# Optimization experiments

Measured on AMD Instinct MI355X. Metric: run time of the kernel, lower is better.

Reference implementation:

```python
import jax, jax.numpy as jnp
import numpy as np

TEMPERATURE = 1.0          # args.matching_temperature default
CONSISTENCY_WEIGHT = 0.5   # args.matching_consistency_weight default
EPS = 1e-6


def setup_inputs() -> dict:
    key = jax.random.key(0)
    k1, k2, k3 = jax.random.split(key, 3)
    query = jax.random.normal(k1, (8192, 1024), dtype=jnp.float32)
    memory_bank = jax.random.normal(k2, (16384, 1024), dtype=jnp.float32)
    # per-memory-entry local density scale (mean kNN distance within the lib)
    neighbor_scale_bank = jax.random.uniform(k3, (16384,), dtype=jnp.float32) + 0.5
    return {
        "query": query,
        "memory_bank": memory_bank,
        "neighbor_scale_bank": neighbor_scale_bank,
        "k": 5,
    }


def _cdist(x, y):
    # Euclidean pairwise distances [Nq, Nm], GEMM-based like torch.cdist.
    x2 = jnp.sum(x * x, axis=1, keepdims=True)          # [Nq, 1]
    y2 = jnp.sum(y * y, axis=1)[None, :]                # [1, Nm]
    d2 = x2 + y2 - 2.0 * (x @ y.T)                      # [Nq, Nm]
    return jnp.sqrt(jnp.maximum(d2, 1e-12))


def reference(query, memory_bank, neighbor_scale_bank, k):
    # _compute_memory_matching_scores with matching_mode='adaptive_knn'
    dist = _cdist(query, memory_bank)                   # [Nq, Nm]
    k = min(k, memory_bank.shape[0])
    neg_d, knn_indices = jax.lax.top_k(-dist, k)        # k smallest distances
    knn_distances = -neg_d                              # [Nq, k]

    # _reduce_knn_distances, mode='adaptive_knn'
    weights = jax.nn.softmax(-knn_distances / TEMPERATURE, axis=1)
    weighted_distance = jnp.sum(weights * knn_distances, axis=1)  # [Nq]

    neighbor_scale = neighbor_scale_bank[knn_indices].mean(axis=1)  # [Nq]
    normalized_distance = weighted_distance / jnp.maximum(neighbor_scale, EPS)

    mean_d = knn_distances.mean(axis=1)
    consistency = knn_distances.std(axis=1) / jnp.maximum(mean_d, EPS)
    return normalized_distance * (1.0 + CONSISTENCY_WEIGHT * consistency)
```

## Files before the change

### kernel.cpp

```cpp
#include <hip/hip_runtime.h>
#include <hip/hip_bf16.h>
#include <math.h>

#define NQ   8192
#define NM   16384
#define DIM  1024
#define KNN  5

#define SPLITS 8
#define SLICE  (NM / SPLITS)
#define TILEM  128
#define TILES  (SLICE / TILEM)
#define BK     64
#define KSTEPS (DIM / BK)
#define UNITS  (TILES * KSTEPS)
#define TPB1   512
#define CPQ    (SPLITS * 16 * 5)

typedef float  f32x4_t  __attribute__((ext_vector_type(4)));
typedef __bf16 bf16x8_t __attribute__((ext_vector_type(8)));

typedef __attribute__((address_space(1))) unsigned int gu32_t;
typedef __attribute__((address_space(3))) unsigned int lu32_t;

__device__ __forceinline__ void gl16(const void* g, void* l) {
    __builtin_amdgcn_global_load_lds((gu32_t*)g, (lu32_t*)l, 16, 0, 0);
}

__global__ void m2_kernel(const float* __restrict__ mem, float* __restrict__ m2) {
    const int row  = blockIdx.x * 4 + (threadIdx.x >> 6);
    const int lane = threadIdx.x & 63;
    const float4* p = reinterpret_cast<const float4*>(mem + (size_t)row * DIM) + lane;
    float s = 0.f;
#pragma unroll
    for (int i = 0; i < 4; ++i) {
        const float4 v = p[i * 64];
        s += v.x * v.x + v.y * v.y + v.z * v.z + v.w * v.w;
    }
#pragma unroll
    for (int off = 32; off > 0; off >>= 1) s += __shfl_down(s, off);
    if (lane == 0) m2[row] = s;
}

__global__ void cvt_bf16_kernel(const float* __restrict__ in,
                                __hip_bfloat16* __restrict__ out, int n8) {
    const int i = blockIdx.x * blockDim.x + threadIdx.x;
    if (i >= n8) return;
    const float4 a = reinterpret_cast<const float4*>(in)[2 * i];
    const float4 b = reinterpret_cast<const float4*>(in)[2 * i + 1];
    bf16x8_t v;
    v[0] = (__bf16)a.x; v[1] = (__bf16)a.y; v[2] = (__bf16)a.z; v[3] = (__bf16)a.w;
    v[4] = (__bf16)b.x; v[5] = (__bf16)b.y; v[6] = (__bf16)b.z; v[7] = (__bf16)b.w;
    reinterpret_cast<bf16x8_t*>(out)[i] = v;
}

__launch_bounds__(TPB1, 4)
__global__ void knn_phase1(const __hip_bfloat16* __restrict__ Qbf,
                           const __hip_bfloat16* __restrict__ Mbf,
                           const float* __restrict__ m2,
                           float* __restrict__ keyws,
                           unsigned short* __restrict__ idxws) {
    __shared__ alignas(16) __bf16 As[2][TILEM][BK];
    __shared__ alignas(16) __bf16 Bs[2][128][BK];
    __shared__ float m2s[SLICE];

    const int t    = threadIdx.x;
    const int lane = t & 63;
    const int wave = t >> 6;
    const int wr   = wave >> 1;
    const int wc   = wave & 1;
    const int g4   = lane >> 4;
    const int l16  = lane & 15;

    const int bid  = blockIdx.x;
    const int qlow = bid & 7;
    const int rest = bid >> 3;
    const int sp   = rest & 7;
    const int qhi  = rest >> 3;
    const int qc   = qhi * 8 + qlow;
    const int q0   = qc * 128;
    const int mbase = sp * SLICE;

#pragma unroll
    for (int i = 0; i < SLICE / TPB1; ++i) m2s[t + i * TPB1] = m2[mbase + t + i * TPB1];

    float    tk[4][5];
    unsigned ti[4][5];
#pragma unroll
    for (int j = 0; j < 4; ++j)
#pragma unroll
        for (int r = 0; r < 5; ++r) { tk[j][r] = 3.4e38f; ti[j][r] = 0u; }

    const int srow = t >> 3;
    const int scol = (((t & 7) ^ (srow & 7)) << 3);
    const int rxa  = l16 & 7;

    f32x4_t acc[2][4];
#pragma unroll
    for (int i = 0; i < 2; ++i)
#pragma unroll
        for (int j = 0; j < 4; ++j) acc[i][j] = {0.f, 0.f, 0.f, 0.f};

    auto stage = [&](int s, int buf) {
        const int tl  = s >> 4;
        const int kk0 = (s & 15) * BK;
        const int rr0 = mbase + tl * TILEM;
        const __hip_bfloat16* ga = Mbf + (size_t)(rr0 + srow) * DIM + kk0 + scol;
        const __hip_bfloat16* gb = Qbf + (size_t)(q0 + srow) * DIM + kk0 + scol;
        char* la = (char*)&As[buf][0][0] + t * 16;
        char* lb = (char*)&Bs[buf][0][0] + t * 16;
        gl16(ga,            la);
        gl16(ga + 64 * DIM, la + 8192);
        gl16(gb,            lb);
        gl16(gb + 64 * DIM, lb + 8192);
    };

    stage(0, 0);
    stage(1, 1);

#pragma unroll 1
    for (int s = 0; s < UNITS; ++s) {
        const int cur = s & 1;

        if (s == UNITS - 1) asm volatile("s_waitcnt vmcnt(0)" ::: "memory");
        else                asm volatile("s_waitcnt vmcnt(4)" ::: "memory");
        __builtin_amdgcn_s_barrier();

        __builtin_amdgcn_s_setprio(1);
#pragma unroll
        for (int kk = 0; kk < BK; kk += 32) {
            const int ch   = (kk >> 3) + g4;
            const int koff = ((ch ^ rxa) << 3);
            const int ar   = wr * 32 + l16;
            const int bc   = wc * 64 + l16;
            const bf16x8_t a0 = *reinterpret_cast<const bf16x8_t*>(&As[cur][ar][koff]);
            const bf16x8_t a1 = *reinterpret_cast<const bf16x8_t*>(&As[cur][ar + 16][koff]);
            const bf16x8_t b0 = *reinterpret_cast<const bf16x8_t*>(&Bs[cur][bc][koff]);
            const bf16x8_t b1 = *reinterpret_cast<const bf16x8_t*>(&Bs[cur][bc + 16][koff]);
            const bf16x8_t b2 = *reinterpret_cast<const bf16x8_t*>(&Bs[cur][bc + 32][koff]);
            const bf16x8_t b3 = *reinterpret_cast<const bf16x8_t*>(&Bs[cur][bc + 48][koff]);
            acc[0][0] = __builtin_amdgcn_mfma_f32_16x16x32_bf16(a0, b0, acc[0][0], 0, 0, 0);
            acc[0][1] = __builtin_amdgcn_mfma_f32_16x16x32_bf16(a0, b1, acc[0][1], 0, 0, 0);
            acc[0][2] = __builtin_amdgcn_mfma_f32_16x16x32_bf16(a0, b2, acc[0][2], 0, 0, 0);
            acc[0][3] = __builtin_amdgcn_mfma_f32_16x16x32_bf16(a0, b3, acc[0][3], 0, 0, 0);
            acc[1][0] = __builtin_amdgcn_mfma_f32_16x16x32_bf16(a1, b0, acc[1][0], 0, 0, 0);
            acc[1][1] = __builtin_amdgcn_mfma_f32_16x16x32_bf16(a1, b1, acc[1][1], 0, 0, 0);
            acc[1][2] = __builtin_amdgcn_mfma_f32_16x16x32_bf16(a1, b2, acc[1][2], 0, 0, 0);
            acc[1][3] = __builtin_amdgcn_mfma_f32_16x16x32_bf16(a1, b3, acc[1][3], 0, 0, 0);
        }
        __builtin_amdgcn_s_setprio(0);

        asm volatile("s_waitcnt lgkmcnt(0)" ::: "memory");
        __builtin_amdgcn_s_barrier();

        if (s + 2 < UNITS) stage(s + 2, cur);

        if ((s & 15) == 15) {
            const int tl = s >> 4;
            const int r0 = mbase + tl * TILEM;
#pragma unroll
            for (int i = 0; i < 2; ++i) {
#pragma unroll
                for (int rg = 0; rg < 4; ++rg) {
                    const int lr = wr * 32 + i * 16 + g4 * 4 + rg;
                    const float mm = m2s[tl * TILEM + lr];
                    const unsigned gidx = (unsigned)(r0 + lr);
#pragma unroll
                    for (int j = 0; j < 4; ++j) {
                        const float key = fmaf(-2.0f, acc[i][j][rg], mm);
                        if (key < tk[j][4]) {
                            tk[j][4] = key; ti[j][4] = gidx;
#pragma unroll
                            for (int ss = 3; ss >= 0; --ss) {
                                const bool sw = tk[j][ss] > tk[j][ss + 1];
                                const float    fa = tk[j][ss], fb = tk[j][ss + 1];
                                const unsigned ia = ti[j][ss], ib = ti[j][ss + 1];
                                tk[j][ss] = sw ? fb : fa; tk[j][ss + 1] = sw ? fa : fb;
                                ti[j][ss] = sw ? ib : ia; ti[j][ss + 1] = sw ? ia : ib;
                            }
                        }
                    }
                }
            }
#pragma unroll
            for (int i = 0; i < 2; ++i)
#pragma unroll
                for (int j = 0; j < 4; ++j) acc[i][j] = {0.f, 0.f, 0.f, 0.f};
        }
    }

#pragma unroll
    for (int j = 0; j < 4; ++j) {
        const int col = wc * 64 + j * 16 + l16;
        const size_t base = (size_t)(q0 + col) * CPQ + sp * 80 + (wr * 4 + g4) * 5;
#pragma unroll
        for (int r = 0; r < 5; ++r) {
            keyws[base + r] = tk[j][r];
            idxws[base + r] = (unsigned short)ti[j][r];
        }
    }
}

__global__ void knn_phase2(const float* __restrict__ query,
                           const float* __restrict__ mem,
                           const float* __restrict__ nsb,
                           const float* __restrict__ keyws,
                           const unsigned short* __restrict__ idxws,
                           float* __restrict__ out) {
    const int wv   = threadIdx.x >> 6;
    const int lane = threadIdx.x & 63;
    const int row  = blockIdx.x * 4 + wv;

    __shared__ int   sel[4][16];
    __shared__ float dsel[4][16];

    float    k[10];
    unsigned id[10];
    const size_t cb = (size_t)row * CPQ;
#pragma unroll
    for (int r = 0; r < 10; ++r) {
        k[r]  = keyws[cb + r * 64 + lane];
        id[r] = (unsigned)idxws[cb + r * 64 + lane];
    }

    for (int rr = 0; rr < 16; ++rr) {
        float lm = k[0];
#pragma unroll
        for (int r = 1; r < 10; ++r) lm = fminf(lm, k[r]);
        float m = lm;
#pragma unroll
        for (int off = 32; off > 0; off >>= 1) m = fminf(m, __shfl_xor(m, off));
        const unsigned long long bal = __ballot(lm == m);
        const bool win = (lane == (int)(__ffsll((long long)bal) - 1));
        unsigned sid = 0; bool done = false;
#pragma unroll
        for (int r = 0; r < 10; ++r) {
            const bool c = win && !done && (k[r] == m);
            sid  = c ? id[r] : sid;
            k[r] = c ? 3.4e38f : k[r];
            done = done || c;
        }
        if (win) sel[wv][rr] = (int)sid;
    }
    __syncthreads();

    const int c = lane >> 2, sub = lane & 3;
    const int mi = sel[wv][c];
    const float4* qp = reinterpret_cast<const float4*>(query + (size_t)row * DIM) + sub * 64;
    const float4* mp = reinterpret_cast<const float4*>(mem + (size_t)mi * DIM) + sub * 64;
    double acc = 0.0;
#pragma unroll 4
    for (int i = 0; i < 64; ++i) {
        const float4 q4 = qp[i];
        const float4 m4 = mp[i];
        const double d0 = (double)q4.x - (double)m4.x;
        const double d1 = (double)q4.y - (double)m4.y;
        const double d2 = (double)q4.z - (double)m4.z;
        const double d3 = (double)q4.w - (double)m4.w;
        acc += d0 * d0 + d1 * d1 + d2 * d2 + d3 * d3;
    }
    acc += __shfl_xor(acc, 1);
    acc += __shfl_xor(acc, 2);
    if (sub == 0) dsel[wv][c] = (float)sqrt(fmax(acc, 1e-12));
    __syncthreads();

    if (lane == 0) {
        float dv[16]; int di[16];
#pragma unroll
        for (int i = 0; i < 16; ++i) { dv[i] = dsel[wv][i]; di[i] = sel[wv][i]; }
        float kd[KNN]; int ki[KNN];
#pragma unroll
        for (int r = 0; r < KNN; ++r) {
            float bv = 3.4e38f; int bi = 0x7fffffff; int bp = -1;
#pragma unroll
            for (int i = 0; i < 16; ++i) {
                const bool better = (dv[i] < bv) || (dv[i] == bv && di[i] < bi);
                if (better) { bv = dv[i]; bi = di[i]; bp = i; }
            }
            kd[r] = bv; ki[r] = bi;
#pragma unroll
            for (int i = 0; i < 16; ++i) if (i == bp) dv[i] = 3.4e38f;
        }
        double dmin = (double)kd[0];
#pragma unroll
        for (int r = 1; r < KNN; ++r) dmin = fmin(dmin, (double)kd[r]);
        double w[KNN], se = 0.0, wd = 0.0, sd = 0.0, sc = 0.0;
#pragma unroll
        for (int r = 0; r < KNN; ++r) {
            w[r] = exp(-((double)kd[r] - dmin));
            se += w[r];
            sd += (double)kd[r];
            sc += (double)nsb[ki[r]];
        }
#pragma unroll
        for (int r = 0; r < KNN; ++r) wd += w[r] * (double)kd[r];
        wd /= se;
        sc /= (double)KNN;
        const double nd   = wd / fmax(sc, 1e-6);
        const double mean = sd / (double)KNN;
        double var = 0.0;
#pragma unroll
        for (int r = 0; r < KNN; ++r) { const double dd = (double)kd[r] - mean; var += dd * dd; }
        var /= (double)KNN;
        const double cons = sqrt(var) / fmax(mean, 1e-6);
        out[row] = (float)(nd * (1.0 + 0.5 * cons));
    }
}

__launch_bounds__(512, 1)
__global__ void fb_knn_phase1(const float* __restrict__ query,
                              const float* __restrict__ mem,
                              const float* __restrict__ m2,
                              float* __restrict__ wkey,
                              int* __restrict__ widx) {
    __shared__ alignas(16) __bf16 Qs[128][72];
    __shared__ alignas(16) __bf16 Ms[128][72];
    __shared__ float D2[128][129];
    __shared__ float m2s[128];

    const int t    = threadIdx.x;
    const int lane = t & 63;
    const int wave = t >> 6;
    const int wr   = wave >> 1;
    const int wc   = wave & 1;

    const int mb    = blockIdx.x & 63;
    const int sp    = blockIdx.x >> 6;
    const int q0    = mb * 128;
    const int mbase = sp * 4096;

    const int srow = t & 127;
    const int sseg = t >> 7;
    const int str = t >> 2;
    const int stc = (t & 3) * 16;

    float topv[8]; int topi[8];
#pragma unroll
    for (int i = 0; i < 8; ++i) { topv[i] = 3.4e38f; topi[i] = 0; }
    float curmax = 3.4e38f;
    const f32x4_t zero = {0.f, 0.f, 0.f, 0.f};

    for (int tile = 0; tile < 32; ++tile) {
        const int c0 = mbase + tile * 128;
        if (t < 128) m2s[t] = m2[c0 + t];
        f32x4_t acc[2][4];
#pragma unroll
        for (int i = 0; i < 2; ++i)
#pragma unroll
            for (int j = 0; j < 4; ++j) acc[i][j] = zero;

        for (int k0 = 0; k0 < DIM; k0 += 64) {
            {
                const float4* qp = reinterpret_cast<const float4*>(query + (size_t)(q0 + str) * DIM + k0 + stc);
                const float4 a0 = qp[0], a1 = qp[1], a2 = qp[2], a3 = qp[3];
                const float4* mp = reinterpret_cast<const float4*>(mem + (size_t)(c0 + str) * DIM + k0 + stc);
                const float4 b0 = mp[0], b1 = mp[1], b2 = mp[2], b3 = mp[3];
                bf16x8_t qa, qb, ma, mbv;
                qa[0] = (__bf16)a0.x; qa[1] = (__bf16)a0.y; qa[2] = (__bf16)a0.z; qa[3] = (__bf16)a0.w;
                qa[4] = (__bf16)a1.x; qa[5] = (__bf16)a1.y; qa[6] = (__bf16)a1.z; qa[7] = (__bf16)a1.w;
                qb[0] = (__bf16)a2.x; qb[1] = (__bf16)a2.y; qb[2] = (__bf16)a2.z; qb[3] = (__bf16)a2.w;
                qb[4] = (__bf16)a3.x; qb[5] = (__bf16)a3.y; qb[6] = (__bf16)a3.z; qb[7] = (__bf16)a3.w;
                ma[0] = (__bf16)b0.x; ma[1] = (__bf16)b0.y; ma[2] = (__bf16)b0.z; ma[3] = (__bf16)b0.w;
                ma[4] = (__bf16)b1.x; ma[5] = (__bf16)b1.y; ma[6] = (__bf16)b1.z; ma[7] = (__bf16)b1.w;
                mbv[0] = (__bf16)b2.x; mbv[1] = (__bf16)b2.y; mbv[2] = (__bf16)b2.z; mbv[3] = (__bf16)b2.w;
                mbv[4] = (__bf16)b3.x; mbv[5] = (__bf16)b3.y; mbv[6] = (__bf16)b3.z; mbv[7] = (__bf16)b3.w;
                *reinterpret_cast<bf16x8_t*>(&Qs[str][stc])     = qa;
                *reinterpret_cast<bf16x8_t*>(&Qs[str][stc + 8]) = qb;
                *reinterpret_cast<bf16x8_t*>(&Ms[str][stc])     = ma;
                *reinterpret_cast<bf16x8_t*>(&Ms[str][stc + 8]) = mbv;
            }
            __syncthreads();
#pragma unroll
            for (int kk = 0; kk < 64; kk += 32) {
                const int koff = kk + ((lane >> 4) << 3);
                const int ar   = wr * 32 + (lane & 15);
                const bf16x8_t a0 = *reinterpret_cast<const bf16x8_t*>(&Qs[ar][koff]);
                const bf16x8_t a1 = *reinterpret_cast<const bf16x8_t*>(&Qs[ar + 16][koff]);
                const int bc = wc * 64 + (lane & 15);
                const bf16x8_t b0 = *reinterpret_cast<const bf16x8_t*>(&Ms[bc][koff]);
                const bf16x8_t b1 = *reinterpret_cast<const bf16x8_t*>(&Ms[bc + 16][koff]);
                const bf16x8_t b2 = *reinterpret_cast<const bf16x8_t*>(&Ms[bc + 32][koff]);
                const bf16x8_t b3 = *reinterpret_cast<const bf16x8_t*>(&Ms[bc + 48][koff]);
                acc[0][0] = __builtin_amdgcn_mfma_f32_16x16x32_bf16(a0, b0, acc[0][0], 0, 0, 0);
                acc[0][1] = __builtin_amdgcn_mfma_f32_16x16x32_bf16(a0, b1, acc[0][1], 0, 0, 0);
                acc[0][2] = __builtin_amdgcn_mfma_f32_16x16x32_bf16(a0, b2, acc[0][2], 0, 0, 0);
                acc[0][3] = __builtin_amdgcn_mfma_f32_16x16x32_bf16(a0, b3, acc[0][3], 0, 0, 0);
                acc[1][0] = __builtin_amdgcn_mfma_f32_16x16x32_bf16(a1, b0, acc[1][0], 0, 0, 0);
                acc[1][1] = __builtin_amdgcn_mfma_f32_16x16x32_bf16(a1, b1, acc[1][1], 0, 0, 0);
                acc[1][2] = __builtin_amdgcn_mfma_f32_16x16x32_bf16(a1, b2, acc[1][2], 0, 0, 0);
                acc[1][3] = __builtin_amdgcn_mfma_f32_16x16x32_bf16(a1, b3, acc[1][3], 0, 0, 0);
            }
            __syncthreads();
        }
#pragma unroll
        for (int i = 0; i < 2; ++i) {
            const int r0 = wr * 32 + i * 16 + ((lane >> 4) << 2);
#pragma unroll
            for (int j = 0; j < 4; ++j) {
                const int cc = wc * 64 + j * 16 + (lane & 15);
                const float mm = m2s[cc];
#pragma unroll
                for (int rg = 0; rg < 4; ++rg)
                    D2[r0 + rg][cc] = mm - 2.0f * acc[i][j][rg];
            }
        }
        __syncthreads();
        {
            const int gbase = c0 + sseg * 32;
#pragma unroll 8
            for (int cc = 0; cc < 32; ++cc) {
                const float key = D2[srow][sseg * 32 + cc];
                if (key < curmax) {
                    bool done = false;
#pragma unroll
                    for (int i = 0; i < 8; ++i) {
                        if (!done && topv[i] == curmax) {
                            topv[i] = key; topi[i] = gbase + cc; done = true;
                        }
                    }
                    curmax = topv[0];
#pragma unroll
                    for (int i = 1; i < 8; ++i) curmax = fmaxf(curmax, topv[i]);
                }
            }
        }
        __syncthreads();
    }
    const size_t base = ((size_t)(q0 + srow) * 4 + sp) * 32 + (size_t)sseg * 8;
#pragma unroll
    for (int j = 0; j < 8; ++j) { wkey[base + j] = topv[j]; widx[base + j] = topi[j]; }
}

__global__ void fb_knn_phase2(const float* __restrict__ query,
                              const float* __restrict__ mem,
                              const float* __restrict__ nsb,
                              const float* __restrict__ wkey,
                              const int* __restrict__ widx,
                              float* __restrict__ out) {
    const int wv   = threadIdx.x >> 6;
    const int lane = threadIdx.x & 63;
    const int row  = blockIdx.x * 4 + wv;
    __shared__ int   sel[4][16];
    __shared__ float dsel[4][16];

    const size_t cb = (size_t)row * 128;
    float k0 = wkey[cb + lane];
    float k1 = wkey[cb + 64 + lane];
    const int i0 = widx[cb + lane];
    const int i1 = widx[cb + 64 + lane];

    for (int r = 0; r < 16; ++r) {
        float m = fminf(k0, k1);
#pragma unroll
        for (int off = 32; off > 0; off >>= 1) m = fminf(m, __shfl_xor(m, off));
        const unsigned long long b0 = __ballot(k0 == m);
        const unsigned long long b1 = __ballot(k1 == m);
        if (b0) {
            if (lane == __ffsll(b0) - 1) { sel[wv][r] = i0; k0 = 3.4e38f; }
        } else {
            if (lane == __ffsll(b1) - 1) { sel[wv][r] = i1; k1 = 3.4e38f; }
        }
    }
    __syncthreads();

    const int c = lane >> 2, sub = lane & 3;
    const int mi = sel[wv][c];
    const float4* qp = reinterpret_cast<const float4*>(query + (size_t)row * DIM) + sub * 64;
    const float4* mp = reinterpret_cast<const float4*>(mem + (size_t)mi * DIM) + sub * 64;
    double acc = 0.0;
#pragma unroll 4
    for (int i = 0; i < 64; ++i) {
        const float4 q4 = qp[i];
        const float4 m4 = mp[i];
        const double d0 = (double)q4.x - (double)m4.x;
        const double d1 = (double)q4.y - (double)m4.y;
        const double d2 = (double)q4.z - (double)m4.z;
        const double d3 = (double)q4.w - (double)m4.w;
        acc += d0 * d0 + d1 * d1 + d2 * d2 + d3 * d3;
    }
    acc += __shfl_xor(acc, 1);
    acc += __shfl_xor(acc, 2);
    if (sub == 0) dsel[wv][c] = (float)sqrt(fmax(acc, 1e-12));
    __syncthreads();

    if (lane == 0) {
        float dv[16]; int di[16];
#pragma unroll
        for (int i = 0; i < 16; ++i) { dv[i] = dsel[wv][i]; di[i] = sel[wv][i]; }
        float kd[KNN]; int ki[KNN];
#pragma unroll
        for (int r = 0; r < KNN; ++r) {
            float bv = 3.4e38f; int bi = 0x7fffffff; int bp = -1;
#pragma unroll
            for (int i = 0; i < 16; ++i) {
                const bool better = (dv[i] < bv) || (dv[i] == bv && di[i] < bi);
                if (better) { bv = dv[i]; bi = di[i]; bp = i; }
            }
            kd[r] = bv; ki[r] = bi;
#pragma unroll
            for (int i = 0; i < 16; ++i) if (i == bp) dv[i] = 3.4e38f;
        }
        double dmin = (double)kd[0];
#pragma unroll
        for (int r = 1; r < KNN; ++r) dmin = fmin(dmin, (double)kd[r]);
        double w[KNN], se = 0.0, wd = 0.0, sd = 0.0, sc = 0.0;
#pragma unroll
        for (int r = 0; r < KNN; ++r) {
            w[r] = exp(-((double)kd[r] - dmin));
            se += w[r];
            sd += (double)kd[r];
            sc += (double)nsb[ki[r]];
        }
#pragma unroll
        for (int r = 0; r < KNN; ++r) wd += w[r] * (double)kd[r];
        wd /= se;
        sc /= (double)KNN;
        const double nd   = wd / fmax(sc, 1e-6);
        const double mean = sd / (double)KNN;
        double var = 0.0;
#pragma unroll
        for (int r = 0; r < KNN; ++r) { const double dd = (double)kd[r] - mean; var += dd * dd; }
        var /= (double)KNN;
        const double cons = sqrt(var) / fmax(mean, 1e-6);
        out[row] = (float)(nd * (1.0 + 0.5 * cons));
    }
}

extern "C" void kernel_launch(void* const* d_in, const int* in_sizes, int n_in,
                              void* d_out, int out_size, void* d_ws, size_t ws_size,
                              hipStream_t stream) {
    const float* query = (const float*)d_in[0];
    const float* mem   = (const float*)d_in[1];
    const float* nsb   = (const float*)d_in[2];
    float* out = (float*)d_out;
    char* ws = (char*)d_ws;

    const size_t offQ   = 0;
    const size_t offM   = offQ + (size_t)NQ * DIM * 2;
    const size_t offm2  = offM + (size_t)NM * DIM * 2;
    const size_t offkey = offm2 + (size_t)NM * 4;
    const size_t offidx = offkey + (size_t)NQ * CPQ * 4;
    const size_t need   = offidx + (size_t)NQ * CPQ * 2;

    if (ws_size >= need) {
        __hip_bfloat16* Qbf = (__hip_bfloat16*)(ws + offQ);
        __hip_bfloat16* Mbf = (__hip_bfloat16*)(ws + offM);
        float*          m2  = (float*)(ws + offm2);
        float*          key = (float*)(ws + offkey);
        unsigned short* idx = (unsigned short*)(ws + offidx);

        hipLaunchKernelGGL(cvt_bf16_kernel, dim3(NQ * DIM / 8 / 256), dim3(256), 0, stream,
                           query, Qbf, NQ * DIM / 8);
        hipLaunchKernelGGL(cvt_bf16_kernel, dim3(NM * DIM / 8 / 256), dim3(256), 0, stream,
                           mem, Mbf, NM * DIM / 8);
        hipLaunchKernelGGL(m2_kernel, dim3(NM / 4), dim3(256), 0, stream, mem, m2);
        hipLaunchKernelGGL(knn_phase1, dim3((NQ / 128) * SPLITS), dim3(TPB1), 0, stream,
                           Qbf, Mbf, m2, key, idx);
        hipLaunchKernelGGL(knn_phase2, dim3(NQ / 4), dim3(256), 0, stream,
                           query, mem, nsb, key, idx, out);
    } else {
        float* wkey = (float*)ws;
        int*   widx = (int*)(ws + (size_t)NQ * 128 * 4);
        float* m2   = (float*)(ws + (size_t)NQ * 128 * 8);
        hipLaunchKernelGGL(m2_kernel, dim3(NM / 4), dim3(256), 0, stream, mem, m2);
        hipLaunchKernelGGL(fb_knn_phase1, dim3((NQ / 128) * 4), dim3(512), 0, stream,
                           query, mem, m2, wkey, widx);
        hipLaunchKernelGGL(fb_knn_phase2, dim3(NQ / 4), dim3(256), 0, stream,
                           query, mem, nsb, wkey, widx, out);
    }
}
```

Measured before the change: 494.9 us.

## Enlarge kNN GEMM block tile to 256x256 and fuse bf16 convert with norms

Phase 1 block tile grows from 128x128 to 256x256, with each wave now computing 128x64 (8x4 MFMA fragments). This raises arithmetic intensity per LDS byte and halves the global reloads of Q and M. The per-query candidate count shrinks accordingly, and phase 2 merges 5 instead of 10 candidates per lane. Separately, the memory-bank bf16 conversion and the squared-norm computation are fused into one kernel so the bank is read once. The cost is more registers, with launch bounds lowered to 2 blocks per CU, double the LDS, and fewer blocks in the grid (256), which may underfill the 256 CUs.

```diff
diff --git a/kernel.cpp b/kernel.cpp
--- a/kernel.cpp
+++ b/kernel.cpp
@@ -9,13 +9,14 @@
 
 #define SPLITS 8
 #define SLICE  (NM / SPLITS)
-#define TILEM  128
-#define TILES  (SLICE / TILEM)
+#define BM     256
+#define BN     256
+#define TILES  (SLICE / BM)
 #define BK     64
 #define KSTEPS (DIM / BK)
 #define UNITS  (TILES * KSTEPS)
 #define TPB1   512
-#define CPQ    (SPLITS * 16 * 5)
+#define CPQ    (SPLITS * 8 * 5)
 
 typedef float  f32x4_t  __attribute__((ext_vector_type(4)));
 typedef __bf16 bf16x8_t __attribute__((ext_vector_type(8)));
@@ -27,15 +28,23 @@
     __builtin_amdgcn_global_load_lds((gu32_t*)g, (lu32_t*)l, 16, 0, 0);
 }
 
-__global__ void m2_kernel(const float* __restrict__ mem, float* __restrict__ m2) {
+__global__ void cvt_m2_kernel(const float* __restrict__ mem,
+                              __hip_bfloat16* __restrict__ out,
+                              float* __restrict__ m2) {
     const int row  = blockIdx.x * 4 + (threadIdx.x >> 6);
     const int lane = threadIdx.x & 63;
-    const float4* p = reinterpret_cast<const float4*>(mem + (size_t)row * DIM) + lane;
+    const float4* p = reinterpret_cast<const float4*>(mem + (size_t)row * DIM + lane * 16);
     float s = 0.f;
 #pragma unroll
-    for (int i = 0; i < 4; ++i) {
-        const float4 v = p[i * 64];
-        s += v.x * v.x + v.y * v.y + v.z * v.z + v.w * v.w;
+    for (int h = 0; h < 2; ++h) {
+        const float4 a = p[2 * h];
+        const float4 b = p[2 * h + 1];
+        bf16x8_t v;
+        v[0] = (__bf16)a.x; v[1] = (__bf16)a.y; v[2] = (__bf16)a.z; v[3] = (__bf16)a.w;
+        v[4] = (__bf16)b.x; v[5] = (__bf16)b.y; v[6] = (__bf16)b.z; v[7] = (__bf16)b.w;
+        reinterpret_cast<bf16x8_t*>(out + (size_t)row * DIM + lane * 16)[h] = v;
+        s += a.x * a.x + a.y * a.y + a.z * a.z + a.w * a.w;
+        s += b.x * b.x + b.y * b.y + b.z * b.z + b.w * b.w;
     }
 #pragma unroll
     for (int off = 32; off > 0; off >>= 1) s += __shfl_down(s, off);
@@ -54,35 +63,39 @@
     reinterpret_cast<bf16x8_t*>(out)[i] = v;
 }
 
-__launch_bounds__(TPB1, 4)
+__launch_bounds__(TPB1, 2)
 __global__ void knn_phase1(const __hip_bfloat16* __restrict__ Qbf,
                            const __hip_bfloat16* __restrict__ Mbf,
                            const float* __restrict__ m2,
                            float* __restrict__ keyws,
                            unsigned short* __restrict__ idxws) {
-    __shared__ alignas(16) __bf16 As[2][TILEM][BK];
-    __shared__ alignas(16) __bf16 Bs[2][128][BK];
+    __shared__ alignas(16) __bf16 As[2][BM][BK];
+    __shared__ alignas(16) __bf16 Bs[2][BN][BK];
     __shared__ float m2s[SLICE];
 
     const int t    = threadIdx.x;
     const int lane = t & 63;
     const int wave = t >> 6;
-    const int wr   = wave >> 1;
-    const int wc   = wave & 1;
+    const int wb   = wave >> 2;
+    const int cb   = wave & 3;
     const int g4   = lane >> 4;
     const int l16  = lane & 15;
 
     const int bid  = blockIdx.x;
-    const int qlow = bid & 7;
-    const int rest = bid >> 3;
-    const int sp   = rest & 7;
-    const int qhi  = rest >> 3;
-    const int qc   = qhi * 8 + qlow;
-    const int q0   = qc * 128;
+    const int sp   = bid & 7;
+    const int qc   = bid >> 3;
+    const int q0   = qc * BN;
     const int mbase = sp * SLICE;
 
-#pragma unroll
-    for (int i = 0; i < SLICE / TPB1; ++i) m2s[t + i * TPB1] = m2[mbase + t + i * TPB1];
+    {
+        float m2r[SLICE / TPB1];
+#pragma unroll
+        for (int i = 0; i < SLICE / TPB1; ++i) m2r[i] = m2[mbase + t + i * TPB1];
+        asm volatile("s_waitcnt vmcnt(0)" ::: "memory");
+#pragma unroll
+        for (int i = 0; i < SLICE / TPB1; ++i) m2s[t + i * TPB1] = m2r[i];
+        __syncthreads();
+    }
 
     float    tk[4][5];
     unsigned ti[4][5];
@@ -95,24 +108,25 @@
     const int scol = (((t & 7) ^ (srow & 7)) << 3);
     const int rxa  = l16 & 7;
 
-    f32x4_t acc[2][4];
-#pragma unroll
-    for (int i = 0; i < 2; ++i)
+    f32x4_t acc[8][4];
+#pragma unroll
+    for (int i = 0; i < 8; ++i)
 #pragma unroll
         for (int j = 0; j < 4; ++j) acc[i][j] = {0.f, 0.f, 0.f, 0.f};
 
     auto stage = [&](int s, int buf) {
         const int tl  = s >> 4;
         const int kk0 = (s & 15) * BK;
-        const int rr0 = mbase + tl * TILEM;
+        const int rr0 = mbase + tl * BM;
         const __hip_bfloat16* ga = Mbf + (size_t)(rr0 + srow) * DIM + kk0 + scol;
         const __hip_bfloat16* gb = Qbf + (size_t)(q0 + srow) * DIM + kk0 + scol;
         char* la = (char*)&As[buf][0][0] + t * 16;
         char* lb = (char*)&Bs[buf][0][0] + t * 16;
-        gl16(ga,            la);
-        gl16(ga + 64 * DIM, la + 8192);
-        gl16(gb,            lb);
-        gl16(gb + 64 * DIM, lb + 8192);
+#pragma unroll
+        for (int h = 0; h < 4; ++h) {
+            gl16(ga + (size_t)(h * 64) * DIM, la + h * 8192);
+            gl16(gb + (size_t)(h * 64) * DIM, lb + h * 8192);
+        }
     };
 
     stage(0, 0);
@@ -123,7 +137,7 @@
         const int cur = s & 1;
 
         if (s == UNITS - 1) asm volatile("s_waitcnt vmcnt(0)" ::: "memory");
-        else                asm volatile("s_waitcnt vmcnt(4)" ::: "memory");
+        else                asm volatile("s_waitcnt vmcnt(8)" ::: "memory");
         __builtin_amdgcn_s_barrier();
 
         __builtin_amdgcn_s_setprio(1);
@@ -131,22 +145,21 @@
         for (int kk = 0; kk < BK; kk += 32) {
             const int ch   = (kk >> 3) + g4;
             const int koff = ((ch ^ rxa) << 3);
-            const int ar   = wr * 32 + l16;
-            const int bc   = wc * 64 + l16;
-            const bf16x8_t a0 = *reinterpret_cast<const bf16x8_t*>(&As[cur][ar][koff]);
-            const bf16x8_t a1 = *reinterpret_cast<const bf16x8_t*>(&As[cur][ar + 16][koff]);
-            const bf16x8_t b0 = *reinterpret_cast<const bf16x8_t*>(&Bs[cur][bc][koff]);
-            const bf16x8_t b1 = *reinterpret_cast<const bf16x8_t*>(&Bs[cur][bc + 16][koff]);
-            const bf16x8_t b2 = *reinterpret_cast<const bf16x8_t*>(&Bs[cur][bc + 32][koff]);
-            const bf16x8_t b3 = *reinterpret_cast<const bf16x8_t*>(&Bs[cur][bc + 48][koff]);
-            acc[0][0] = __builtin_amdgcn_mfma_f32_16x16x32_bf16(a0, b0, acc[0][0], 0, 0, 0);
-            acc[0][1] = __builtin_amdgcn_mfma_f32_16x16x32_bf16(a0, b1, acc[0][1], 0, 0, 0);
-            acc[0][2] = __builtin_amdgcn_mfma_f32_16x16x32_bf16(a0, b2, acc[0][2], 0, 0, 0);
-            acc[0][3] = __builtin_amdgcn_mfma_f32_16x16x32_bf16(a0, b3, acc[0][3], 0, 0, 0);
-            acc[1][0] = __builtin_amdgcn_mfma_f32_16x16x32_bf16(a1, b0, acc[1][0], 0, 0, 0);
-            acc[1][1] = __builtin_amdgcn_mfma_f32_16x16x32_bf16(a1, b1, acc[1][1], 0, 0, 0);
-            acc[1][2] = __builtin_amdgcn_mfma_f32_16x16x32_bf16(a1, b2, acc[1][2], 0, 0, 0);
-            acc[1][3] = __builtin_amdgcn_mfma_f32_16x16x32_bf16(a1, b3, acc[1][3], 0, 0, 0);
+            bf16x8_t bfr[4];
+#pragma unroll
+            for (int jf = 0; jf < 4; ++jf) {
+                const int bc = cb * 64 + jf * 16 + l16;
+                bfr[jf] = *reinterpret_cast<const bf16x8_t*>(&Bs[cur][bc][koff]);
+            }
+#pragma unroll
+            for (int rf = 0; rf < 8; ++rf) {
+                const int ar = wb * 128 + rf * 16 + l16;
+                const bf16x8_t a = *reinterpret_cast<const bf16x8_t*>(&As[cur][ar][koff]);
+                acc[rf][0] = __builtin_amdgcn_mfma_f32_16x16x32_bf16(a, bfr[0], acc[rf][0], 0, 0, 0);
+                acc[rf][1] = __builtin_amdgcn_mfma_f32_16x16x32_bf16(a, bfr[1], acc[rf][1], 0, 0, 0);
+                acc[rf][2] = __builtin_amdgcn_mfma_f32_16x16x32_bf16(a, bfr[2], acc[rf][2], 0, 0, 0);
+                acc[rf][3] = __builtin_amdgcn_mfma_f32_16x16x32_bf16(a, bfr[3], acc[rf][3], 0, 0, 0);
+            }
         }
         __builtin_amdgcn_s_setprio(0);
 
@@ -157,17 +170,17 @@
 
         if ((s & 15) == 15) {
             const int tl = s >> 4;
-            const int r0 = mbase + tl * TILEM;
-#pragma unroll
-            for (int i = 0; i < 2; ++i) {
+            const int r0 = mbase + tl * BM;
+#pragma unroll
+            for (int rf = 0; rf < 8; ++rf) {
 #pragma unroll
                 for (int rg = 0; rg < 4; ++rg) {
-                    const int lr = wr * 32 + i * 16 + g4 * 4 + rg;
-                    const float mm = m2s[tl * TILEM + lr];
+                    const int lr = wb * 128 + rf * 16 + g4 * 4 + rg;
+                    const float mm = m2s[tl * BM + lr];
                     const unsigned gidx = (unsigned)(r0 + lr);
 #pragma unroll
                     for (int j = 0; j < 4; ++j) {
-                        const float key = fmaf(-2.0f, acc[i][j][rg], mm);
+                        const float key = fmaf(-2.0f, acc[rf][j][rg], mm);
                         if (key < tk[j][4]) {
                             tk[j][4] = key; ti[j][4] = gidx;
 #pragma unroll
@@ -183,7 +196,7 @@
                 }
             }
 #pragma unroll
-            for (int i = 0; i < 2; ++i)
+            for (int i = 0; i < 8; ++i)
 #pragma unroll
                 for (int j = 0; j < 4; ++j) acc[i][j] = {0.f, 0.f, 0.f, 0.f};
         }
@@ -191,8 +204,8 @@
 
 #pragma unroll
     for (int j = 0; j < 4; ++j) {
-        const int col = wc * 64 + j * 16 + l16;
-        const size_t base = (size_t)(q0 + col) * CPQ + sp * 80 + (wr * 4 + g4) * 5;
+        const int col = cb * 64 + j * 16 + l16;
+        const size_t base = (size_t)(q0 + col) * CPQ + sp * 40 + (wb * 4 + g4) * 5;
 #pragma unroll
         for (int r = 0; r < 5; ++r) {
             keyws[base + r] = tk[j][r];
@@ -214,11 +227,11 @@
     __shared__ int   sel[4][16];
     __shared__ float dsel[4][16];
 
-    float    k[10];
-    unsigned id[10];
+    float    k[5];
+    unsigned id[5];
     const size_t cb = (size_t)row * CPQ;
 #pragma unroll
-    for (int r = 0; r < 10; ++r) {
+    for (int r = 0; r < 5; ++r) {
         k[r]  = keyws[cb + r * 64 + lane];
         id[r] = (unsigned)idxws[cb + r * 64 + lane];
     }
@@ -226,7 +239,7 @@
     for (int rr = 0; rr < 16; ++rr) {
         float lm = k[0];
 #pragma unroll
-        for (int r = 1; r < 10; ++r) lm = fminf(lm, k[r]);
+        for (int r = 1; r < 5; ++r) lm = fminf(lm, k[r]);
         float m = lm;
 #pragma unroll
         for (int off = 32; off > 0; off >>= 1) m = fminf(m, __shfl_xor(m, off));
@@ -234,7 +247,7 @@
         const bool win = (lane == (int)(__ffsll((long long)bal) - 1));
         unsigned sid = 0; bool done = false;
 #pragma unroll
-        for (int r = 0; r < 10; ++r) {
+        for (int r = 0; r < 5; ++r) {
             const bool c = win && !done && (k[r] == m);
             sid  = c ? id[r] : sid;
             k[r] = c ? 3.4e38f : k[r];
@@ -307,6 +320,23 @@
     }
 }
 
+typedef float f32x4fb_t __attribute__((ext_vector_type(4)));
+
+__global__ void fb_m2_kernel(const float* __restrict__ mem, float* __restrict__ m2) {
+    const int row  = blockIdx.x * 4 + (threadIdx.x >> 6);
+    const int lane = threadIdx.x & 63;
+    const float4* p = reinterpret_cast<const float4*>(mem + (size_t)row * DIM) + lane;
+    float s = 0.f;
+#pragma unroll
+    for (int i = 0; i < 4; ++i) {
+        const float4 v = p[i * 64];
+        s += v.x * v.x + v.y * v.y + v.z * v.z + v.w * v.w;
+    }
+#pragma unroll
+    for (int off = 32; off > 0; off >>= 1) s += __shfl_down(s, off);
+    if (lane == 0) m2[row] = s;
+}
+
 __launch_bounds__(512, 1)
 __global__ void fb_knn_phase1(const float* __restrict__ query,
                               const float* __restrict__ mem,
@@ -338,12 +368,12 @@
 #pragma unroll
     for (int i = 0; i < 8; ++i) { topv[i] = 3.4e38f; topi[i] = 0; }
     float curmax = 3.4e38f;
-    const f32x4_t zero = {0.f, 0.f, 0.f, 0.f};
+    const f32x4fb_t zero = {0.f, 0.f, 0.f, 0.f};
 
     for (int tile = 0; tile < 32; ++tile) {
         const int c0 = mbase + tile * 128;
         if (t < 128) m2s[t] = m2[c0 + t];
-        f32x4_t acc[2][4];
+        f32x4fb_t acc[2][4];
 #pragma unroll
         for (int i = 0; i < 2; ++i)
 #pragma unroll
@@ -551,10 +581,8 @@
 
         hipLaunchKernelGGL(cvt_bf16_kernel, dim3(NQ * DIM / 8 / 256), dim3(256), 0, stream,
                            query, Qbf, NQ * DIM / 8);
-        hipLaunchKernelGGL(cvt_bf16_kernel, dim3(NM * DIM / 8 / 256), dim3(256), 0, stream,
-                           mem, Mbf, NM * DIM / 8);
-        hipLaunchKernelGGL(m2_kernel, dim3(NM / 4), dim3(256), 0, stream, mem, m2);
-        hipLaunchKernelGGL(knn_phase1, dim3((NQ / 128) * SPLITS), dim3(TPB1), 0, stream,
+        hipLaunchKernelGGL(cvt_m2_kernel, dim3(NM / 4), dim3(256), 0, stream, mem, Mbf, m2);
+        hipLaunchKernelGGL(knn_phase1, dim3((NQ / BN) * SPLITS), dim3(TPB1), 0, stream,
                            Qbf, Mbf, m2, key, idx);
         hipLaunchKernelGGL(knn_phase2, dim3(NQ / 4), dim3(256), 0, stream,
                            query, mem, nsb, key, idx, out);
@@ -562,7 +590,7 @@
         float* wkey = (float*)ws;
         int*   widx = (int*)(ws + (size_t)NQ * 128 * 4);
         float* m2   = (float*)(ws + (size_t)NQ * 128 * 8);
-        hipLaunchKernelGGL(m2_kernel, dim3(NM / 4), dim3(256), 0, stream, mem, m2);
+        hipLaunchKernelGGL(fb_m2_kernel, dim3(NM / 4), dim3(256), 0, stream, mem, m2);
         hipLaunchKernelGGL(fb_knn_phase1, dim3((NQ / 128) * 4), dim3(512), 0, stream,
                            query, mem, m2, wkey, widx);
         hipLaunchKernelGGL(fb_knn_phase2, dim3(NQ / 4), dim3(256), 0, stream,
```

New measurement: 638.5 us. 1.29x slower.
